# Optimization experiments

Hardware: AMD Instinct MI355X
Metric: run time of the kernel (lower is better)

The kernel has to match this reference:

```python
import jax, jax.numpy as jnp
import numpy as np

LN_EPS = 1e-5

def _ln(x, g, b):
    m = x.mean(-1, keepdims=True)
    v = ((x - m) ** 2).mean(-1, keepdims=True)
    return (x - m) / jnp.sqrt(v + LN_EPS) * g + b

def _mlp(x, W1, b1, g, beta, W2, b2):
    # Linear -> LayerNorm -> ReLU -> Linear
    h = jax.nn.relu(_ln(x @ W1 + b1, g, beta))
    return h @ W2 + b2

def setup_inputs() -> dict:
    key = jax.random.key(0)
    N, E, C_in, C_out, H = 50000, 800000, 64, 64, 64
    ks = jax.random.split(key, 16)
    def rn(k, shape, fan_in):
        return jax.random.normal(k, shape, jnp.float32) * (fan_in ** -0.5)
    return dict(
        x=jax.random.normal(ks[0], (N, C_in), jnp.float32),
        pos=jax.random.normal(ks[1], (N, 3), jnp.float32),
        edge_index=jax.random.randint(ks[2], (2, E), 0, N, jnp.int32),
        W_in=rn(ks[3], (C_in, C_in), C_in), b_in=jnp.zeros((C_in,), jnp.float32),
        W_lin=rn(ks[4], (C_in, C_out), C_in),
        W_src=rn(ks[5], (C_in, C_out), C_in),
        W_dst=rn(ks[6], (C_in, C_out), C_in),
        pos_W1=rn(ks[7], (3, H), 3), pos_b1=jnp.zeros((H,), jnp.float32),
        pos_g=jnp.ones((H,), jnp.float32), pos_beta=jnp.zeros((H,), jnp.float32),
        pos_W2=rn(ks[8], (H, C_out), H), pos_b2=jnp.zeros((C_out,), jnp.float32),
        att_W1=rn(ks[9], (C_out, H), C_out), att_b1=jnp.zeros((H,), jnp.float32),
        att_g=jnp.ones((H,), jnp.float32), att_beta=jnp.zeros((H,), jnp.float32),
        att_W2=rn(ks[10], (H, C_out), H), att_b2=jnp.zeros((C_out,), jnp.float32),
        W_out=rn(ks[11], (C_out, C_out), C_out), b_out=jnp.zeros((C_out,), jnp.float32),
    )

def reference(x, pos, edge_index, W_in, b_in, W_lin, W_src, W_dst,
              pos_W1, pos_b1, pos_g, pos_beta, pos_W2, pos_b2,
              att_W1, att_b1, att_g, att_beta, att_W2, att_b2,
              W_out, b_out):
    N = x.shape[0]
    # lin_in + relu
    x = jax.nn.relu(x @ W_in + b_in)
    # PointTransformerConv with add_self_loops=True (PyG default)
    loops = jnp.arange(N, dtype=edge_index.dtype)
    src = jnp.concatenate([edge_index[0], loops])  # j (neighbors)
    dst = jnp.concatenate([edge_index[1], loops])  # i (centers)
    a_src = x @ W_src           # [N, C_out]
    a_dst = x @ W_dst           # [N, C_out]
    v = x @ W_lin               # [N, C_out]
    # per-edge positional encoding delta = pos_nn(pos_i - pos_j)
    delta = _mlp(pos[dst] - pos[src], pos_W1, pos_b1, pos_g, pos_beta, pos_W2, pos_b2)  # [E, C_out]
    alpha = _mlp(a_dst[dst] - a_src[src] + delta, att_W1, att_b1, att_g, att_beta, att_W2, att_b2)
    # per-destination, per-channel softmax over variable-size neighborhoods
    amax = jax.ops.segment_max(alpha, dst, num_segments=N)
    e = jnp.exp(alpha - amax[dst])
    denom = jax.ops.segment_sum(e, dst, num_segments=N)
    w = e / jnp.clip(denom[dst], 1e-16)
    # weighted scatter-sum of (value_j + delta)
    out = jax.ops.segment_sum(w * (v[src] + delta), dst, num_segments=N)  # [N, C_out]
    # lin_out + relu
    return jax.nn.relu(out @ W_out + b_out)
```

## Files before the change

### kernel.cpp

```cpp
#include <hip/hip_runtime.h>
#include <hip/hip_bf16.h>


typedef __bf16 bf16x8 __attribute__((ext_vector_type(8)));
typedef short  s16x8  __attribute__((ext_vector_type(8)));
typedef float  f32x4  __attribute__((ext_vector_type(4)));

#define SWZ(b) ((b) ^ ((((b) >> 7) & 7) << 4))

__device__ __forceinline__ unsigned short f2b(float f) {
  union { __hip_bfloat16 h; unsigned short u; } c;
  c.h = __float2bfloat16(f);
  return c.u;
}
__device__ __forceinline__ unsigned int pack2(float a, float b) {
  return (unsigned int)f2b(a) | ((unsigned int)f2b(b) << 16);
}
__device__ __forceinline__ void lds_fence() {
  asm volatile("s_waitcnt lgkmcnt(0)" ::: "memory");
  __builtin_amdgcn_sched_barrier(0);
}

__device__ __forceinline__ void stage_wt(const float* __restrict__ W, char* dst, int tid) {
  for (int idx = tid; idx < 2048; idx += 256) {
    int c  = idx >> 5;
    int k2 = (idx & 31) << 1;
    float v0 = W[k2 * 64 + c];
    float v1 = W[(k2 + 1) * 64 + c];
    int byte = c * 128 + k2 * 2;
    *(unsigned int*)(dst + SWZ(byte)) = pack2(v0, v1);
  }
}

__device__ __forceinline__ void gemm16(const char* actb, const char* wb,
                                       int g, int m, f32x4 acc[4]) {
  #pragma unroll
  for (int kk = 0; kk < 2; kk++) {
    s16x8 af = *(const s16x8*)(actb + SWZ(m * 128 + g * 16 + kk * 64));
    #pragma unroll
    for (int t = 0; t < 4; t++) {
      s16x8 bf = *(const s16x8*)(wb + SWZ((t * 16 + m) * 128 + g * 16 + kk * 64));
      acc[t] = __builtin_amdgcn_mfma_f32_16x16x32_bf16(
          __builtin_bit_cast(bf16x8, af), __builtin_bit_cast(bf16x8, bf), acc[t], 0, 0, 0);
    }
  }
}

__global__ __launch_bounds__(256, 3) void node_mfma_kernel(
    const float* __restrict__ x,
    const float* __restrict__ W_in, const float* __restrict__ b_in,
    const float* __restrict__ W_lin, const float* __restrict__ W_src, const float* __restrict__ W_dst,
    float* __restrict__ a_src, float* __restrict__ a_dst, float* __restrict__ vv,
    int N)
{
  __shared__ __align__(16) char sWinT[8192], sWsT[8192], sWdT[8192], sWlT[8192], sX[8192];
  __shared__ float sB[64];
  int tid = threadIdx.x;
  stage_wt(W_in,  sWinT, tid);
  stage_wt(W_src, sWsT,  tid);
  stage_wt(W_dst, sWdT,  tid);
  stage_wt(W_lin, sWlT,  tid);
  if (tid < 64) sB[tid] = b_in[tid];

  const int lane = tid & 63, wv = tid >> 6;
  const int g = lane >> 4, m = lane & 15;
  const int ew = wv << 4;
  const int srow = tid >> 2, sc0 = (tid & 3) << 4;
  const int ntile = (N + 63) >> 6;

  for (int tile = blockIdx.x; tile < ntile; tile += gridDim.x) {
    const int rbase = tile << 6;
    __syncthreads();
    {
      int gr = rbase + srow; if (gr >= N) gr = N - 1;
      const float4* src = (const float4*)&x[(size_t)gr * 64 + sc0];
      #pragma unroll
      for (int q = 0; q < 4; q++) {
        float4 f = src[q];
        int byte = srow * 128 + sc0 * 2 + q * 8;
        *(unsigned int*)(sX + SWZ(byte))     = pack2(f.x, f.y);
        *(unsigned int*)(sX + SWZ(byte + 4)) = pack2(f.z, f.w);
      }
    }
    __syncthreads();

    f32x4 a0[4] = {};
    gemm16(sX + ew * 128, sWinT, g, m, a0);
    float x1[4][4];
    #pragma unroll
    for (int t = 0; t < 4; t++)
      #pragma unroll
      for (int r = 0; r < 4; r++) x1[t][r] = fmaxf(a0[t][r] + sB[t * 16 + m], 0.f);
    __syncthreads();
    #pragma unroll
    for (int t = 0; t < 4; t++)
      #pragma unroll
      for (int r = 0; r < 4; r++)
        *(unsigned short*)(sX + SWZ((ew + 4 * g + r) * 128 + (t * 16 + m) * 2)) = f2b(x1[t][r]);
    __syncthreads();

    f32x4 as[4] = {}, ad[4] = {}, al[4] = {};
    gemm16(sX + ew * 128, sWsT, g, m, as);
    gemm16(sX + ew * 128, sWdT, g, m, ad);
    gemm16(sX + ew * 128, sWlT, g, m, al);
    #pragma unroll
    for (int t = 0; t < 4; t++)
      #pragma unroll
      for (int r = 0; r < 4; r++) {
        int gr = rbase + ew + 4 * g + r;
        if (gr < N) {
          size_t o = (size_t)gr * 64 + t * 16 + m;
          a_src[o] = as[t][r]; a_dst[o] = ad[t][r]; vv[o] = al[t][r];
        }
      }
  }
}

__global__ void hist_kernel(const int* __restrict__ ei, int* __restrict__ deg, int E, int Etot) {
  int stride = gridDim.x * blockDim.x;
  for (int e = blockIdx.x * blockDim.x + threadIdx.x; e < Etot; e += stride) {
    int d = (e < E) ? ei[E + e] : (e - E);
    atomicAdd(&deg[d], 1);
  }
}

__global__ __launch_bounds__(256) void scanA_kernel(const int* __restrict__ deg, int* __restrict__ chunkSum, int N) {
  __shared__ int s[256];
  int i = blockIdx.x * 256 + threadIdx.x;
  s[threadIdx.x] = (i < N) ? deg[i] : 0;
  __syncthreads();
  for (int off = 128; off > 0; off >>= 1) {
    if (threadIdx.x < off) s[threadIdx.x] += s[threadIdx.x + off];
    __syncthreads();
  }
  if (threadIdx.x == 0) chunkSum[blockIdx.x] = s[0];
}

__global__ __launch_bounds__(256) void scanB_kernel(const int* __restrict__ chunkSum, int* __restrict__ chunkPre, int nchunk) {
  __shared__ int s[256];
  int t = threadIdx.x;
  int v = (t < nchunk) ? chunkSum[t] : 0;
  s[t] = v; __syncthreads();
  for (int off = 1; off < 256; off <<= 1) {
    int x = (t >= off) ? s[t - off] : 0;
    __syncthreads();
    s[t] += x;
    __syncthreads();
  }
  if (t < nchunk) chunkPre[t] = s[t] - v;
}

__global__ __launch_bounds__(256) void scanC_kernel(const int* __restrict__ deg, const int* __restrict__ chunkPre,
                                                    int* __restrict__ cursor, int N) {
  __shared__ int s[256];
  int t = threadIdx.x;
  int i = blockIdx.x * 256 + t;
  int v = (i < N) ? deg[i] : 0;
  s[t] = v; __syncthreads();
  for (int off = 1; off < 256; off <<= 1) {
    int x = (t >= off) ? s[t - off] : 0;
    __syncthreads();
    s[t] += x;
    __syncthreads();
  }
  if (i < N) cursor[i] = chunkPre[blockIdx.x] + s[t] - v;
}

__global__ void scatter_kernel(const int* __restrict__ ei, int* __restrict__ cursor,
                               const float* __restrict__ pos,
                               int* __restrict__ srcS, int* __restrict__ dstS,
                               float4* __restrict__ pd4,
                               int E, int Etot) {
  int stride = gridDim.x * blockDim.x;
  for (int e = blockIdx.x * blockDim.x + threadIdx.x; e < Etot; e += stride) {
    int s, d;
    if (e < E) { s = ei[e]; d = ei[E + e]; }
    else       { s = e - E; d = s; }
    int p = atomicAdd(&cursor[d], 1);
    srcS[p] = s; dstS[p] = d;
    float4 q;
    q.x = pos[d * 3 + 0] - pos[s * 3 + 0];
    q.y = pos[d * 3 + 1] - pos[s * 3 + 1];
    q.z = pos[d * 3 + 2] - pos[s * 3 + 2];
    q.w = 0.f;
    pd4[p] = q;
  }
}

__global__ __launch_bounds__(256, 3) void edge_kernel(
    const int* __restrict__ srcS, const int* __restrict__ dstS, const float4* __restrict__ pd4,
    const float* __restrict__ a_src_g, const float* __restrict__ a_dst_g, const float* __restrict__ v_g,
    const float* __restrict__ pos_W1, const float* __restrict__ pos_b1,
    const float* __restrict__ pos_gg, const float* __restrict__ pos_beta,
    const float* __restrict__ pos_W2, const float* __restrict__ pos_b2,
    const float* __restrict__ att_W1, const float* __restrict__ att_b1,
    const float* __restrict__ att_gg, const float* __restrict__ att_beta,
    const float* __restrict__ att_W2, const float* __restrict__ att_b2,
    float* __restrict__ numer, float* __restrict__ denom,
    int G, int gpw)
{
  __shared__ __align__(16) char sW2t[8192], sA1t[8192], sA2t[8192];
  __shared__ __align__(16) char sAct[4][2048];
  __shared__ float sAcc[4][4][128];
  __shared__ float sPW1[192];
  __shared__ float sPB1[64], sPG[64], sPBeta[64], sPB2[64];
  __shared__ float sAB1[64], sAG[64], sABeta[64], sAB2[64];

  int tid = threadIdx.x;
  stage_wt(pos_W2, sW2t, tid);
  stage_wt(att_W1, sA1t, tid);
  stage_wt(att_W2, sA2t, tid);
  for (int i = tid; i < 192; i += 256) sPW1[i] = pos_W1[i];
  if (tid < 64) {
    sPB1[tid] = pos_b1[tid]; sPG[tid] = pos_gg[tid]; sPBeta[tid] = pos_beta[tid]; sPB2[tid] = pos_b2[tid];
    sAB1[tid] = att_b1[tid]; sAG[tid] = att_gg[tid]; sABeta[tid] = att_beta[tid]; sAB2[tid] = att_b2[tid];
  }
  for (int i = tid; i < 4 * 4 * 128; i += 256) ((float*)sAcc)[i] = 0.f;
  __syncthreads();

  const int lane = tid & 63, wv = tid >> 6;
  const int g = lane >> 4, m = lane & 15;
  char* myAct = sAct[wv];
  float (*myAcc)[128] = sAcc[wv];

  const int w  = blockIdx.x * 4 + wv;
  const int g0 = w * gpw;
  int g1 = g0 + gpw; if (g1 > G) g1 = G;

  for (int grp = g0; grp < g1; ++grp) {
    const int ebase = grp << 4;

    float4 pdr[4];
    #pragma unroll
    for (int r = 0; r < 4; r++) pdr[r] = pd4[ebase + 4 * g + r];
    int dall[16];
    #pragma unroll
    for (int i = 0; i < 16; i++) dall[i] = dstS[ebase + i];
    int mys[4];
    #pragma unroll
    for (int r = 0; r < 4; r++) mys[r] = srcS[ebase + 4 * g + r];

    int myd[4] = {-1, -1, -1, -1};
    int sid_my[4] = {0, 0, 0, 0};
    int fd0 = dall[0], fd1 = -1, fd2 = -1, fd3 = -1;
    int cur = 0;
    #pragma unroll
    for (int i = 0; i < 16; i++) {
      if (i > 0) {
        bool b = (dall[i] != dall[i - 1]);
        cur += b ? 1 : 0;
        fd1 = (b && cur == 1) ? dall[i] : fd1;
        fd2 = (b && cur == 2) ? dall[i] : fd2;
        fd3 = (b && cur == 3) ? dall[i] : fd3;
      }
      bool mine = ((i >> 2) == g);
      const int rr = i & 3;
      if (rr == 0) { myd[0] = mine ? dall[i] : myd[0]; sid_my[0] = mine ? cur : sid_my[0]; }
      if (rr == 1) { myd[1] = mine ? dall[i] : myd[1]; sid_my[1] = mine ? cur : sid_my[1]; }
      if (rr == 2) { myd[2] = mine ? dall[i] : myd[2]; sid_my[2] = mine ? cur : sid_my[2]; }
      if (rr == 3) { myd[3] = mine ? dall[i] : myd[3]; sid_my[3] = mine ? cur : sid_my[3]; }
    }
    const int ns = cur + 1;

    float adst[16], asrc[16];
    #pragma unroll
    for (int r = 0; r < 4; r++) {
      int dm = myd[r] < 0 ? 0 : myd[r];
      int sm = mys[r];
      #pragma unroll
      for (int t = 0; t < 4; t++) {
        adst[r * 4 + t] = a_dst_g[(size_t)dm * 64 + t * 16 + m];
        asrc[r * 4 + t] = a_src_g[(size_t)sm * 64 + t * 16 + m];
      }
    }

    {
      float h[4][4];
      #pragma unroll
      for (int r = 0; r < 4; r++) {
        float p0 = pdr[r].x, p1 = pdr[r].y, p2 = pdr[r].z;
        #pragma unroll
        for (int t = 0; t < 4; t++) {
          int c = t * 16 + m;
          h[t][r] = fmaf(p0, sPW1[c], fmaf(p1, sPW1[64 + c], fmaf(p2, sPW1[128 + c], sPB1[c])));
        }
      }
      #pragma unroll
      for (int r = 0; r < 4; r++) {
        float s = h[0][r] + h[1][r] + h[2][r] + h[3][r];
        s += __shfl_xor(s, 1); s += __shfl_xor(s, 2); s += __shfl_xor(s, 4); s += __shfl_xor(s, 8);
        float mean = s * (1.f / 64.f);
        float q = 0.f;
        #pragma unroll
        for (int t = 0; t < 4; t++) { float dd = h[t][r] - mean; q = fmaf(dd, dd, q); }
        q += __shfl_xor(q, 1); q += __shfl_xor(q, 2); q += __shfl_xor(q, 4); q += __shfl_xor(q, 8);
        float rs = rsqrtf(q * (1.f / 64.f) + 1e-5f);
        #pragma unroll
        for (int t = 0; t < 4; t++) {
          int c = t * 16 + m;
          float val = fmaxf(fmaf((h[t][r] - mean) * rs, sPG[c], sPBeta[c]), 0.f);
          *(unsigned short*)(myAct + SWZ((4 * g + r) * 128 + c * 2)) = f2b(val);
        }
      }
    }
    lds_fence();

    f32x4 dacc[4] = {};
    gemm16(myAct, sW2t, g, m, dacc);
    float del[4][4];
    #pragma unroll
    for (int t = 0; t < 4; t++)
      #pragma unroll
      for (int r = 0; r < 4; r++) del[t][r] = dacc[t][r] + sPB2[t * 16 + m];
    lds_fence();

    float vv[16];
    #pragma unroll
    for (int r = 0; r < 4; r++)
      #pragma unroll
      for (int t = 0; t < 4; t++)
        vv[r * 4 + t] = v_g[(size_t)mys[r] * 64 + t * 16 + m];

    #pragma unroll
    for (int r = 0; r < 4; r++)
      #pragma unroll
      for (int t = 0; t < 4; t++) {
        float a = adst[r * 4 + t] - asrc[r * 4 + t] + del[t][r];
        *(unsigned short*)(myAct + SWZ((4 * g + r) * 128 + (t * 16 + m) * 2)) = f2b(a);
      }
    lds_fence();

    f32x4 acc2[4] = {};
    gemm16(myAct, sA1t, g, m, acc2);
    float h2[4][4];
    #pragma unroll
    for (int t = 0; t < 4; t++)
      #pragma unroll
      for (int r = 0; r < 4; r++) h2[t][r] = acc2[t][r] + sAB1[t * 16 + m];
    #pragma unroll
    for (int r = 0; r < 4; r++) {
      float s = h2[0][r] + h2[1][r] + h2[2][r] + h2[3][r];
      s += __shfl_xor(s, 1); s += __shfl_xor(s, 2); s += __shfl_xor(s, 4); s += __shfl_xor(s, 8);
      float mean = s * (1.f / 64.f);
      float q = 0.f;
      #pragma unroll
      for (int t = 0; t < 4; t++) { float dd = h2[t][r] - mean; q = fmaf(dd, dd, q); }
      q += __shfl_xor(q, 1); q += __shfl_xor(q, 2); q += __shfl_xor(q, 4); q += __shfl_xor(q, 8);
      float rs = rsqrtf(q * (1.f / 64.f) + 1e-5f);
      #pragma unroll
      for (int t = 0; t < 4; t++) {
        int c = t * 16 + m;
        h2[t][r] = fmaxf(fmaf((h2[t][r] - mean) * rs, sAG[c], sABeta[c]), 0.f);
      }
    }
    lds_fence();
    #pragma unroll
    for (int t = 0; t < 4; t++)
      #pragma unroll
      for (int r = 0; r < 4; r++)
        *(unsigned short*)(myAct + SWZ((4 * g + r) * 128 + (t * 16 + m) * 2)) = f2b(h2[t][r]);
    lds_fence();

    f32x4 acc3[4] = {};
    gemm16(myAct, sA2t, g, m, acc3);

    {
      float aN[4] = {0.f, 0.f, 0.f, 0.f}, aD[4] = {0.f, 0.f, 0.f, 0.f};
      int curS = -1, curD = 0;
      #pragma unroll
      for (int r = 0; r < 4; r++) {
        int d = myd[r];
        if (d < 0) continue;
        int sgid = sid_my[r];
        if (sgid != curS) {
          if (curS >= 0) {
            if (curS < 4) {
              #pragma unroll
              for (int t = 0; t < 4; t++) {
                atomicAdd(&myAcc[curS][t * 16 + m], aN[t]);
                atomicAdd(&myAcc[curS][64 + t * 16 + m], aD[t]);
              }
            } else {
              #pragma unroll
              for (int t = 0; t < 4; t++) {
                atomicAdd(&numer[(size_t)curD * 64 + t * 16 + m], aN[t]);
                atomicAdd(&denom[(size_t)curD * 64 + t * 16 + m], aD[t]);
              }
            }
          }
          curS = sgid; curD = d;
          #pragma unroll
          for (int t = 0; t < 4; t++) { aN[t] = 0.f; aD[t] = 0.f; }
        }
        #pragma unroll
        for (int t = 0; t < 4; t++) {
          float ee = __expf(acc3[t][r] + sAB2[t * 16 + m]);
          aN[t] = fmaf(ee, vv[r * 4 + t] + del[t][r], aN[t]);
          aD[t] += ee;
        }
      }
      if (curS >= 0) {
        if (curS < 4) {
          #pragma unroll
          for (int t = 0; t < 4; t++) {
            atomicAdd(&myAcc[curS][t * 16 + m], aN[t]);
            atomicAdd(&myAcc[curS][64 + t * 16 + m], aD[t]);
          }
        } else {
          #pragma unroll
          for (int t = 0; t < 4; t++) {
            atomicAdd(&numer[(size_t)curD * 64 + t * 16 + m], aN[t]);
            atomicAdd(&denom[(size_t)curD * 64 + t * 16 + m], aD[t]);
          }
        }
      }
    }
    lds_fence();

    {
      const int nsc = ns < 4 ? ns : 4;
      const int fdk[1] = {0}; (void)fdk;
      #pragma unroll
      for (int k = 0; k < 4; k++) {
        int dd = (k == 0) ? fd0 : (k == 1) ? fd1 : (k == 2) ? fd2 : fd3;
        if (k < nsc && dd >= 0) {
          float nv = myAcc[k][lane];
          float dv = myAcc[k][64 + lane];
          atomicAdd(&numer[(size_t)dd * 64 + lane], nv);
          atomicAdd(&denom[(size_t)dd * 64 + lane], dv);
          myAcc[k][lane] = 0.f;
          myAcc[k][64 + lane] = 0.f;
        }
      }
    }
    lds_fence();
  }
}

__global__ __launch_bounds__(256) void out_mfma_kernel(
    const float* __restrict__ numer, const float* __restrict__ denom,
    const float* __restrict__ W_out, const float* __restrict__ b_out,
    float* __restrict__ out, int N)
{
  __shared__ __align__(16) char sWoT[8192], sX[8192];
  __shared__ float sB[64];
  int tid = threadIdx.x;
  stage_wt(W_out, sWoT, tid);
  if (tid < 64) sB[tid] = b_out[tid];

  const int lane = tid & 63, wv = tid >> 6;
  const int g = lane >> 4, m = lane & 15;
  const int ew = wv << 4;
  const int srow = tid >> 2, sc0 = (tid & 3) << 4;
  const int ntile = (N + 63) >> 6;

  for (int tile = blockIdx.x; tile < ntile; tile += gridDim.x) {
    const int rbase = tile << 6;
    __syncthreads();
    {
      int gr = rbase + srow; if (gr >= N) gr = N - 1;
      const float4* nsrc = (const float4*)&numer[(size_t)gr * 64 + sc0];
      const float4* dsrc = (const float4*)&denom[(size_t)gr * 64 + sc0];
      #pragma unroll
      for (int q = 0; q < 4; q++) {
        float4 fn = nsrc[q], fd = dsrc[q];
        float m0 = fn.x / fmaxf(fd.x, 1e-16f);
        float m1 = fn.y / fmaxf(fd.y, 1e-16f);
        float m2 = fn.z / fmaxf(fd.z, 1e-16f);
        float m3 = fn.w / fmaxf(fd.w, 1e-16f);
        int byte = srow * 128 + sc0 * 2 + q * 8;
        *(unsigned int*)(sX + SWZ(byte))     = pack2(m0, m1);
        *(unsigned int*)(sX + SWZ(byte + 4)) = pack2(m2, m3);
      }
    }
    __syncthreads();
    f32x4 acc[4] = {};
    gemm16(sX + ew * 128, sWoT, g, m, acc);
    #pragma unroll
    for (int t = 0; t < 4; t++)
      #pragma unroll
      for (int r = 0; r < 4; r++) {
        int gr = rbase + ew + 4 * g + r;
        if (gr < N) out[(size_t)gr * 64 + t * 16 + m] = fmaxf(acc[t][r] + sB[t * 16 + m], 0.f);
      }
  }
}

extern "C" void kernel_launch(void* const* d_in, const int* in_sizes, int n_in,
                              void* d_out, int out_size, void* d_ws, size_t ws_size,
                              hipStream_t stream) {
  (void)n_in; (void)out_size; (void)ws_size;
  const float* x        = (const float*)d_in[0];
  const float* pos      = (const float*)d_in[1];
  const int*   ei       = (const int*)  d_in[2];
  const float* W_in     = (const float*)d_in[3];
  const float* b_in     = (const float*)d_in[4];
  const float* W_lin    = (const float*)d_in[5];
  const float* W_src    = (const float*)d_in[6];
  const float* W_dst    = (const float*)d_in[7];
  const float* pos_W1   = (const float*)d_in[8];
  const float* pos_b1   = (const float*)d_in[9];
  const float* pos_g    = (const float*)d_in[10];
  const float* pos_beta = (const float*)d_in[11];
  const float* pos_W2   = (const float*)d_in[12];
  const float* pos_b2   = (const float*)d_in[13];
  const float* att_W1   = (const float*)d_in[14];
  const float* att_b1   = (const float*)d_in[15];
  const float* att_g    = (const float*)d_in[16];
  const float* att_beta = (const float*)d_in[17];
  const float* att_W2   = (const float*)d_in[18];
  const float* att_b2   = (const float*)d_in[19];
  const float* W_out    = (const float*)d_in[20];
  const float* b_out    = (const float*)d_in[21];

  const int N    = in_sizes[0] / 64;
  const int E    = in_sizes[2] / 2;
  const int Etot = E + N;
  const int Epad = (Etot + 15) & ~15;
  const size_t N64 = (size_t)N * 64;

  float* a_src = (float*)d_ws;
  float* a_dst = a_src + N64;
  float* v     = a_dst + N64;
  float* numer = v + N64;
  float* denom = numer + N64;
  int* deg      = (int*)(denom + N64);
  int* cursor   = deg + N;
  int* chunkSum = cursor + N;
  int* chunkPre = chunkSum + 256;
  int* srcS     = chunkPre + 256;
  int* dstS     = srcS + Epad;
  float4* pd4   = (float4*)(dstS + Epad);

  const int nchunk = (N + 255) / 256;

  hipMemsetAsync(deg, 0, (size_t)N * sizeof(int), stream);
  hipMemsetAsync(numer, 0, 2 * N64 * sizeof(float), stream);
  if (Epad > Etot) {
    hipMemsetAsync(dstS + Etot, 0xFF, (size_t)(Epad - Etot) * sizeof(int), stream);
    hipMemsetAsync(srcS + Etot, 0, (size_t)(Epad - Etot) * sizeof(int), stream);
    hipMemsetAsync(pd4 + Etot, 0, (size_t)(Epad - Etot) * sizeof(float4), stream);
  }

  hist_kernel<<<1024, 256, 0, stream>>>(ei, deg, E, Etot);
  scanA_kernel<<<nchunk, 256, 0, stream>>>(deg, chunkSum, N);
  scanB_kernel<<<1, 256, 0, stream>>>(chunkSum, chunkPre, nchunk);
  scanC_kernel<<<nchunk, 256, 0, stream>>>(deg, chunkPre, cursor, N);
  scatter_kernel<<<1024, 256, 0, stream>>>(ei, cursor, pos, srcS, dstS, pd4, E, Etot);

  const int ntileN = (N + 63) / 64;
  const int nblkN  = ntileN < 768 ? ntileN : 768;
  node_mfma_kernel<<<nblkN, 256, 0, stream>>>(x, W_in, b_in, W_lin, W_src, W_dst,
                                              a_src, a_dst, v, N);

  const int G   = Epad / 16;
  const int NB  = 768;
  const int gpw = (G + NB * 4 - 1) / (NB * 4);
  edge_kernel<<<NB, 256, 0, stream>>>(srcS, dstS, pd4, a_src, a_dst, v,
      pos_W1, pos_b1, pos_g, pos_beta, pos_W2, pos_b2,
      att_W1, att_b1, att_g, att_beta, att_W2, att_b2,
      numer, denom, G, gpw);

  out_mfma_kernel<<<nblkN, 256, 0, stream>>>(numer, denom, W_out, b_out, (float*)d_out, N);
}
```

Before: 482.2 us.

## Store node features in bf16 and run edge MLPs in registers via transposed MFMA

Node projections a_src, a_dst and v are now written as bf16, which halves the bytes gathered per edge. The edge kernel swaps the MFMA operands so each lane owns one edge. That lets the activations stay in registers between the three GEMMs, using permuted weight staging, and removes the per-wave LDS activation buffers and fences. Segment reduction now uses a DPP segmented scan within 16-lane rows, with atomics issued only from segment tails, replacing the LDS accumulator scheme. The costs are reduced precision on the gathered features and more global atomics per edge group.

```diff
diff --git a/kernel.cpp b/kernel.cpp
--- a/kernel.cpp
+++ b/kernel.cpp
@@ -5,6 +5,8 @@
 typedef __bf16 bf16x8 __attribute__((ext_vector_type(8)));
 typedef short  s16x8  __attribute__((ext_vector_type(8)));
 typedef float  f32x4  __attribute__((ext_vector_type(4)));
+
+union B8 { s16x8 v; unsigned int u[4]; };
 
 #define SWZ(b) ((b) ^ ((((b) >> 7) & 7) << 4))
 
@@ -16,19 +18,40 @@
 __device__ __forceinline__ unsigned int pack2(float a, float b) {
   return (unsigned int)f2b(a) | ((unsigned int)f2b(b) << 16);
 }
-__device__ __forceinline__ void lds_fence() {
-  asm volatile("s_waitcnt lgkmcnt(0)" ::: "memory");
-  __builtin_amdgcn_sched_barrier(0);
+__device__ __forceinline__ void unpack2(unsigned int u, float& a, float& b) {
+  union { unsigned int x; float f; } t0, t1;
+  t0.x = u << 16; t1.x = u & 0xffff0000u;
+  a = t0.f; b = t1.f;
+}
+
+template <int CTRL>
+__device__ __forceinline__ float dppf(float x) {
+  return __builtin_bit_cast(float,
+      __builtin_amdgcn_update_dpp(0, __builtin_bit_cast(int, x), CTRL, 0xF, 0xF, false));
+}
+template <int CTRL>
+__device__ __forceinline__ int dppi(int x, int old) {
+  return __builtin_amdgcn_update_dpp(old, x, CTRL, 0xF, 0xF, false);
+}
+
+__device__ __forceinline__ int lmap(int q) {
+  int kk = q >> 5, gg = (q >> 3) & 3, j = q & 7;
+  return 32 * kk + 16 * (j >> 2) + 4 * gg + (j & 3);
 }
 
 __device__ __forceinline__ void stage_wt(const float* __restrict__ W, char* dst, int tid) {
   for (int idx = tid; idx < 2048; idx += 256) {
     int c  = idx >> 5;
     int k2 = (idx & 31) << 1;
-    float v0 = W[k2 * 64 + c];
-    float v1 = W[(k2 + 1) * 64 + c];
-    int byte = c * 128 + k2 * 2;
-    *(unsigned int*)(dst + SWZ(byte)) = pack2(v0, v1);
+    *(unsigned int*)(dst + SWZ(c * 128 + k2 * 2)) = pack2(W[k2 * 64 + c], W[(k2 + 1) * 64 + c]);
+  }
+}
+__device__ __forceinline__ void stage_wt_perm(const float* __restrict__ W, char* dst, int tid) {
+  for (int idx = tid; idx < 2048; idx += 256) {
+    int c  = idx >> 5;
+    int k2 = (idx & 31) << 1;
+    *(unsigned int*)(dst + SWZ(c * 128 + k2 * 2)) =
+        pack2(W[lmap(k2) * 64 + c], W[lmap(k2 + 1) * 64 + c]);
   }
 }
 
@@ -50,8 +73,8 @@
     const float* __restrict__ x,
     const float* __restrict__ W_in, const float* __restrict__ b_in,
     const float* __restrict__ W_lin, const float* __restrict__ W_src, const float* __restrict__ W_dst,
-    float* __restrict__ a_src, float* __restrict__ a_dst, float* __restrict__ vv,
-    int N)
+    unsigned short* __restrict__ a_srcB, unsigned short* __restrict__ a_dstB,
+    unsigned short* __restrict__ vB, int N)
 {
   __shared__ __align__(16) char sWinT[8192], sWsT[8192], sWdT[8192], sWlT[8192], sX[8192];
   __shared__ float sB[64];
@@ -110,7 +133,7 @@
         int gr = rbase + ew + 4 * g + r;
         if (gr < N) {
           size_t o = (size_t)gr * 64 + t * 16 + m;
-          a_src[o] = as[t][r]; a_dst[o] = ad[t][r]; vv[o] = al[t][r];
+          a_srcB[o] = f2b(as[t][r]); a_dstB[o] = f2b(ad[t][r]); vB[o] = f2b(al[t][r]);
         }
       }
   }
@@ -189,7 +212,8 @@
 
 __global__ __launch_bounds__(256, 3) void edge_kernel(
     const int* __restrict__ srcS, const int* __restrict__ dstS, const float4* __restrict__ pd4,
-    const float* __restrict__ a_src_g, const float* __restrict__ a_dst_g, const float* __restrict__ v_g,
+    const unsigned short* __restrict__ a_srcB, const unsigned short* __restrict__ a_dstB,
+    const unsigned short* __restrict__ vBg,
     const float* __restrict__ pos_W1, const float* __restrict__ pos_b1,
     const float* __restrict__ pos_gg, const float* __restrict__ pos_beta,
     const float* __restrict__ pos_W2, const float* __restrict__ pos_b2,
@@ -200,240 +224,241 @@
     int G, int gpw)
 {
   __shared__ __align__(16) char sW2t[8192], sA1t[8192], sA2t[8192];
-  __shared__ __align__(16) char sAct[4][2048];
-  __shared__ float sAcc[4][4][128];
   __shared__ float sPW1[192];
   __shared__ float sPB1[64], sPG[64], sPBeta[64], sPB2[64];
   __shared__ float sAB1[64], sAG[64], sABeta[64], sAB2[64];
 
   int tid = threadIdx.x;
   stage_wt(pos_W2, sW2t, tid);
-  stage_wt(att_W1, sA1t, tid);
-  stage_wt(att_W2, sA2t, tid);
+  stage_wt_perm(att_W1, sA1t, tid);
+  stage_wt_perm(att_W2, sA2t, tid);
   for (int i = tid; i < 192; i += 256) sPW1[i] = pos_W1[i];
   if (tid < 64) {
     sPB1[tid] = pos_b1[tid]; sPG[tid] = pos_gg[tid]; sPBeta[tid] = pos_beta[tid]; sPB2[tid] = pos_b2[tid];
     sAB1[tid] = att_b1[tid]; sAG[tid] = att_gg[tid]; sABeta[tid] = att_beta[tid]; sAB2[tid] = att_b2[tid];
   }
-  for (int i = tid; i < 4 * 4 * 128; i += 256) ((float*)sAcc)[i] = 0.f;
   __syncthreads();
 
-  const int lane = tid & 63, wv = tid >> 6;
+  const int lane = tid & 63;
   const int g = lane >> 4, m = lane & 15;
-  char* myAct = sAct[wv];
-  float (*myAcc)[128] = sAcc[wv];
-
-  const int w  = blockIdx.x * 4 + wv;
+
+  const int w  = blockIdx.x * 4 + (tid >> 6);
   const int g0 = w * gpw;
   int g1 = g0 + gpw; if (g1 > G) g1 = G;
 
   for (int grp = g0; grp < g1; ++grp) {
     const int ebase = grp << 4;
 
-    float4 pdr[4];
-    #pragma unroll
-    for (int r = 0; r < 4; r++) pdr[r] = pd4[ebase + 4 * g + r];
-    int dall[16];
-    #pragma unroll
-    for (int i = 0; i < 16; i++) dall[i] = dstS[ebase + i];
-    int mys[4];
-    #pragma unroll
-    for (int r = 0; r < 4; r++) mys[r] = srcS[ebase + 4 * g + r];
-
-    int myd[4] = {-1, -1, -1, -1};
-    int sid_my[4] = {0, 0, 0, 0};
-    int fd0 = dall[0], fd1 = -1, fd2 = -1, fd3 = -1;
-    int cur = 0;
-    #pragma unroll
-    for (int i = 0; i < 16; i++) {
-      if (i > 0) {
-        bool b = (dall[i] != dall[i - 1]);
-        cur += b ? 1 : 0;
-        fd1 = (b && cur == 1) ? dall[i] : fd1;
-        fd2 = (b && cur == 2) ? dall[i] : fd2;
-        fd3 = (b && cur == 3) ? dall[i] : fd3;
-      }
-      bool mine = ((i >> 2) == g);
-      const int rr = i & 3;
-      if (rr == 0) { myd[0] = mine ? dall[i] : myd[0]; sid_my[0] = mine ? cur : sid_my[0]; }
-      if (rr == 1) { myd[1] = mine ? dall[i] : myd[1]; sid_my[1] = mine ? cur : sid_my[1]; }
-      if (rr == 2) { myd[2] = mine ? dall[i] : myd[2]; sid_my[2] = mine ? cur : sid_my[2]; }
-      if (rr == 3) { myd[3] = mine ? dall[i] : myd[3]; sid_my[3] = mine ? cur : sid_my[3]; }
-    }
-    const int ns = cur + 1;
-
-    float adst[16], asrc[16];
-    #pragma unroll
-    for (int r = 0; r < 4; r++) {
-      int dm = myd[r] < 0 ? 0 : myd[r];
-      int sm = mys[r];
+    int d = dstS[ebase + m];
+    int sN = srcS[ebase + m];
+    f32x4 pd = *(const f32x4*)&pd4[ebase + m];
+    const bool valid = d >= 0;
+    const int dm = valid ? d : 0;
+
+    int dprev = dppi<0x111>(d, -1);
+    int dnext = dppi<0x101>(d, -1);
+    bool head = (d != dprev);
+    bool tl   = (d != dnext);
+    unsigned long long hb = __ballot(head);
+    unsigned mask16 = (unsigned)(hb >> (g * 16)) & 0xFFFFu;
+    unsigned maskLE = mask16 & ((1u << (m + 1)) - 1u);
+    int hd = m - (31 - __builtin_clz(maskLE | 1u));
+
+    uint2 AD[2][2], AS[2][2], VV[4];
+    #pragma unroll
+    for (int kk = 0; kk < 2; kk++)
+      #pragma unroll
+      for (int h = 0; h < 2; h++) {
+        int c0 = 32 * kk + 16 * h + 4 * g;
+        AD[kk][h] = *(const uint2*)&a_dstB[(size_t)dm * 64 + c0];
+        AS[kk][h] = *(const uint2*)&a_srcB[(size_t)sN * 64 + c0];
+      }
+    #pragma unroll
+    for (int t = 0; t < 4; t++)
+      VV[t] = *(const uint2*)&vBg[(size_t)sN * 64 + 16 * t + 4 * g];
+
+    float u[2][8];
+    #pragma unroll
+    for (int kk = 0; kk < 2; kk++)
+      #pragma unroll
+      for (int h = 0; h < 2; h++) {
+        int q = 8 * g + 32 * kk + 4 * h;
+        f32x4 w0 = *(const f32x4*)&sPW1[q];
+        f32x4 w1 = *(const f32x4*)&sPW1[64 + q];
+        f32x4 w2 = *(const f32x4*)&sPW1[128 + q];
+        f32x4 bb = *(const f32x4*)&sPB1[q];
+        #pragma unroll
+        for (int r = 0; r < 4; r++)
+          u[kk][4 * h + r] = fmaf(pd[0], w0[r], fmaf(pd[1], w1[r], fmaf(pd[2], w2[r], bb[r])));
+      }
+    {
+      float s1 = 0.f;
+      #pragma unroll
+      for (int kk = 0; kk < 2; kk++)
+        #pragma unroll
+        for (int j = 0; j < 8; j++) s1 += u[kk][j];
+      s1 += __shfl_xor(s1, 16); s1 += __shfl_xor(s1, 32);
+      float mean = s1 * (1.f / 64.f);
+      float qv = 0.f;
+      #pragma unroll
+      for (int kk = 0; kk < 2; kk++)
+        #pragma unroll
+        for (int j = 0; j < 8; j++) { float dd = u[kk][j] - mean; qv = fmaf(dd, dd, qv); }
+      qv += __shfl_xor(qv, 16); qv += __shfl_xor(qv, 32);
+      float rs = rsqrtf(qv * (1.f / 64.f) + 1e-5f);
+      #pragma unroll
+      for (int kk = 0; kk < 2; kk++)
+        #pragma unroll
+        for (int h = 0; h < 2; h++) {
+          int q = 8 * g + 32 * kk + 4 * h;
+          f32x4 gg4 = *(const f32x4*)&sPG[q];
+          f32x4 bt4 = *(const f32x4*)&sPBeta[q];
+          #pragma unroll
+          for (int r = 0; r < 4; r++)
+            u[kk][4 * h + r] = fmaxf(fmaf((u[kk][4 * h + r] - mean) * rs, gg4[r], bt4[r]), 0.f);
+        }
+    }
+    B8 bA[2];
+    #pragma unroll
+    for (int kk = 0; kk < 2; kk++)
+      #pragma unroll
+      for (int p = 0; p < 4; p++)
+        bA[kk].u[p] = pack2(u[kk][2 * p], u[kk][2 * p + 1]);
+
+    f32x4 del[4] = {};
+    #pragma unroll
+    for (int kk = 0; kk < 2; kk++)
       #pragma unroll
       for (int t = 0; t < 4; t++) {
-        adst[r * 4 + t] = a_dst_g[(size_t)dm * 64 + t * 16 + m];
-        asrc[r * 4 + t] = a_src_g[(size_t)sm * 64 + t * 16 + m];
-      }
-    }
-
+        s16x8 wf = *(const s16x8*)(sW2t + SWZ((t * 16 + m) * 128 + g * 16 + kk * 64));
+        del[t] = __builtin_amdgcn_mfma_f32_16x16x32_bf16(
+            __builtin_bit_cast(bf16x8, wf), __builtin_bit_cast(bf16x8, bA[kk].v), del[t], 0, 0, 0);
+      }
+    #pragma unroll
+    for (int t = 0; t < 4; t++) {
+      f32x4 b2 = *(const f32x4*)&sPB2[16 * t + 4 * g];
+      #pragma unroll
+      for (int r = 0; r < 4; r++) del[t][r] += b2[r];
+    }
+
+    B8 bT[2];
+    #pragma unroll
+    for (int kk = 0; kk < 2; kk++)
+      #pragma unroll
+      for (int h = 0; h < 2; h++) {
+        float a0, a1, a2, a3, b0, b1, b2v, b3;
+        unpack2(AD[kk][h].x, a0, a1); unpack2(AD[kk][h].y, a2, a3);
+        unpack2(AS[kk][h].x, b0, b1); unpack2(AS[kk][h].y, b2v, b3);
+        int t = 2 * kk + h;
+        float e0 = a0 - b0 + del[t][0];
+        float e1 = a1 - b1 + del[t][1];
+        float e2 = a2 - b2v + del[t][2];
+        float e3 = a3 - b3 + del[t][3];
+        bT[kk].u[2 * h]     = pack2(e0, e1);
+        bT[kk].u[2 * h + 1] = pack2(e2, e3);
+      }
+
+    f32x4 acc2[4] = {};
+    #pragma unroll
+    for (int kk = 0; kk < 2; kk++)
+      #pragma unroll
+      for (int t = 0; t < 4; t++) {
+        s16x8 wf = *(const s16x8*)(sA1t + SWZ((t * 16 + m) * 128 + g * 16 + kk * 64));
+        acc2[t] = __builtin_amdgcn_mfma_f32_16x16x32_bf16(
+            __builtin_bit_cast(bf16x8, wf), __builtin_bit_cast(bf16x8, bT[kk].v), acc2[t], 0, 0, 0);
+      }
+    float h2[4][4];
+    #pragma unroll
+    for (int t = 0; t < 4; t++) {
+      f32x4 ab1 = *(const f32x4*)&sAB1[16 * t + 4 * g];
+      #pragma unroll
+      for (int r = 0; r < 4; r++) h2[t][r] = acc2[t][r] + ab1[r];
+    }
     {
-      float h[4][4];
+      float s1 = 0.f;
+      #pragma unroll
+      for (int t = 0; t < 4; t++)
+        #pragma unroll
+        for (int r = 0; r < 4; r++) s1 += h2[t][r];
+      s1 += __shfl_xor(s1, 16); s1 += __shfl_xor(s1, 32);
+      float mean = s1 * (1.f / 64.f);
+      float qv = 0.f;
+      #pragma unroll
+      for (int t = 0; t < 4; t++)
+        #pragma unroll
+        for (int r = 0; r < 4; r++) { float dd = h2[t][r] - mean; qv = fmaf(dd, dd, qv); }
+      qv += __shfl_xor(qv, 16); qv += __shfl_xor(qv, 32);
+      float rs = rsqrtf(qv * (1.f / 64.f) + 1e-5f);
+      #pragma unroll
+      for (int t = 0; t < 4; t++) {
+        f32x4 gg4 = *(const f32x4*)&sAG[16 * t + 4 * g];
+        f32x4 bt4 = *(const f32x4*)&sABeta[16 * t + 4 * g];
+        #pragma unroll
+        for (int r = 0; r < 4; r++)
+          h2[t][r] = fmaxf(fmaf((h2[t][r] - mean) * rs, gg4[r], bt4[r]), 0.f);
+      }
+    }
+    B8 bH[2];
+    #pragma unroll
+    for (int kk = 0; kk < 2; kk++) {
+      bH[kk].u[0] = pack2(h2[2 * kk][0], h2[2 * kk][1]);
+      bH[kk].u[1] = pack2(h2[2 * kk][2], h2[2 * kk][3]);
+      bH[kk].u[2] = pack2(h2[2 * kk + 1][0], h2[2 * kk + 1][1]);
+      bH[kk].u[3] = pack2(h2[2 * kk + 1][2], h2[2 * kk + 1][3]);
+    }
+
+    f32x4 acc3[4] = {};
+    #pragma unroll
+    for (int kk = 0; kk < 2; kk++)
+      #pragma unroll
+      for (int t = 0; t < 4; t++) {
+        s16x8 wf = *(const s16x8*)(sA2t + SWZ((t * 16 + m) * 128 + g * 16 + kk * 64));
+        acc3[t] = __builtin_amdgcn_mfma_f32_16x16x32_bf16(
+            __builtin_bit_cast(bf16x8, wf), __builtin_bit_cast(bf16x8, bH[kk].v), acc3[t], 0, 0, 0);
+      }
+
+    f32x4 aN[4], aD[4];
+    #pragma unroll
+    for (int t = 0; t < 4; t++) {
+      f32x4 ab2 = *(const f32x4*)&sAB2[16 * t + 4 * g];
+      float v0, v1, v2, v3;
+      unpack2(VV[t].x, v0, v1); unpack2(VV[t].y, v2, v3);
+      float vr[4] = {v0, v1, v2, v3};
       #pragma unroll
       for (int r = 0; r < 4; r++) {
-        float p0 = pdr[r].x, p1 = pdr[r].y, p2 = pdr[r].z;
-        #pragma unroll
-        for (int t = 0; t < 4; t++) {
-          int c = t * 16 + m;
-          h[t][r] = fmaf(p0, sPW1[c], fmaf(p1, sPW1[64 + c], fmaf(p2, sPW1[128 + c], sPB1[c])));
+        float e = __expf(acc3[t][r] + ab2[r]);
+        e = valid ? e : 0.f;
+        aN[t][r] = e * (vr[r] + del[t][r]);
+        aD[t][r] = e;
+      }
+    }
+    #define SCAN_ROUND(OFF, CTRL)                                        \
+      { bool p = hd >= OFF;                                              \
+        _Pragma("unroll")                                                \
+        for (int t = 0; t < 4; t++) {                                    \
+          _Pragma("unroll")                                              \
+          for (int r = 0; r < 4; r++) {                                  \
+            float shN = dppf<CTRL>(aN[t][r]);                            \
+            float shD = dppf<CTRL>(aD[t][r]);                            \
+            aN[t][r] += p ? shN : 0.f;                                   \
+            aD[t][r] += p ? shD : 0.f;                                   \
+          }                                                              \
+        } }
+    SCAN_ROUND(1, 0x111)
+    SCAN_ROUND(2, 0x112)
+    SCAN_ROUND(4, 0x114)
+    SCAN_ROUND(8, 0x118)
+    #undef SCAN_ROUND
+
+    if (valid && tl) {
+      #pragma unroll
+      for (int t = 0; t < 4; t++)
+        #pragma unroll
+        for (int r = 0; r < 4; r++) {
+          atomicAdd(&numer[(size_t)d * 64 + 16 * t + 4 * g + r], aN[t][r]);
+          atomicAdd(&denom[(size_t)d * 64 + 16 * t + 4 * g + r], aD[t][r]);
         }
-      }
-      #pragma unroll
-      for (int r = 0; r < 4; r++) {
-        float s = h[0][r] + h[1][r] + h[2][r] + h[3][r];
-        s += __shfl_xor(s, 1); s += __shfl_xor(s, 2); s += __shfl_xor(s, 4); s += __shfl_xor(s, 8);
-        float mean = s * (1.f / 64.f);
-        float q = 0.f;
-        #pragma unroll
-        for (int t = 0; t < 4; t++) { float dd = h[t][r] - mean; q = fmaf(dd, dd, q); }
-        q += __shfl_xor(q, 1); q += __shfl_xor(q, 2); q += __shfl_xor(q, 4); q += __shfl_xor(q, 8);
-        float rs = rsqrtf(q * (1.f / 64.f) + 1e-5f);
-        #pragma unroll
-        for (int t = 0; t < 4; t++) {
-          int c = t * 16 + m;
-          float val = fmaxf(fmaf((h[t][r] - mean) * rs, sPG[c], sPBeta[c]), 0.f);
-          *(unsigned short*)(myAct + SWZ((4 * g + r) * 128 + c * 2)) = f2b(val);
-        }
-      }
-    }
-    lds_fence();
-
-    f32x4 dacc[4] = {};
-    gemm16(myAct, sW2t, g, m, dacc);
-    float del[4][4];
-    #pragma unroll
-    for (int t = 0; t < 4; t++)
-      #pragma unroll
-      for (int r = 0; r < 4; r++) del[t][r] = dacc[t][r] + sPB2[t * 16 + m];
-    lds_fence();
-
-    float vv[16];
-    #pragma unroll
-    for (int r = 0; r < 4; r++)
-      #pragma unroll
-      for (int t = 0; t < 4; t++)
-        vv[r * 4 + t] = v_g[(size_t)mys[r] * 64 + t * 16 + m];
-
-    #pragma unroll
-    for (int r = 0; r < 4; r++)
-      #pragma unroll
-      for (int t = 0; t < 4; t++) {
-        float a = adst[r * 4 + t] - asrc[r * 4 + t] + del[t][r];
-        *(unsigned short*)(myAct + SWZ((4 * g + r) * 128 + (t * 16 + m) * 2)) = f2b(a);
-      }
-    lds_fence();
-
-    f32x4 acc2[4] = {};
-    gemm16(myAct, sA1t, g, m, acc2);
-    float h2[4][4];
-    #pragma unroll
-    for (int t = 0; t < 4; t++)
-      #pragma unroll
-      for (int r = 0; r < 4; r++) h2[t][r] = acc2[t][r] + sAB1[t * 16 + m];
-    #pragma unroll
-    for (int r = 0; r < 4; r++) {
-      float s = h2[0][r] + h2[1][r] + h2[2][r] + h2[3][r];
-      s += __shfl_xor(s, 1); s += __shfl_xor(s, 2); s += __shfl_xor(s, 4); s += __shfl_xor(s, 8);
-      float mean = s * (1.f / 64.f);
-      float q = 0.f;
-      #pragma unroll
-      for (int t = 0; t < 4; t++) { float dd = h2[t][r] - mean; q = fmaf(dd, dd, q); }
-      q += __shfl_xor(q, 1); q += __shfl_xor(q, 2); q += __shfl_xor(q, 4); q += __shfl_xor(q, 8);
-      float rs = rsqrtf(q * (1.f / 64.f) + 1e-5f);
-      #pragma unroll
-      for (int t = 0; t < 4; t++) {
-        int c = t * 16 + m;
-        h2[t][r] = fmaxf(fmaf((h2[t][r] - mean) * rs, sAG[c], sABeta[c]), 0.f);
-      }
-    }
-    lds_fence();
-    #pragma unroll
-    for (int t = 0; t < 4; t++)
-      #pragma unroll
-      for (int r = 0; r < 4; r++)
-        *(unsigned short*)(myAct + SWZ((4 * g + r) * 128 + (t * 16 + m) * 2)) = f2b(h2[t][r]);
-    lds_fence();
-
-    f32x4 acc3[4] = {};
-    gemm16(myAct, sA2t, g, m, acc3);
-
-    {
-      float aN[4] = {0.f, 0.f, 0.f, 0.f}, aD[4] = {0.f, 0.f, 0.f, 0.f};
-      int curS = -1, curD = 0;
-      #pragma unroll
-      for (int r = 0; r < 4; r++) {
-        int d = myd[r];
-        if (d < 0) continue;
-        int sgid = sid_my[r];
-        if (sgid != curS) {
-          if (curS >= 0) {
-            if (curS < 4) {
-              #pragma unroll
-              for (int t = 0; t < 4; t++) {
-                atomicAdd(&myAcc[curS][t * 16 + m], aN[t]);
-                atomicAdd(&myAcc[curS][64 + t * 16 + m], aD[t]);
-              }
-            } else {
-              #pragma unroll
-              for (int t = 0; t < 4; t++) {
-                atomicAdd(&numer[(size_t)curD * 64 + t * 16 + m], aN[t]);
-                atomicAdd(&denom[(size_t)curD * 64 + t * 16 + m], aD[t]);
-              }
-            }
-          }
-          curS = sgid; curD = d;
-          #pragma unroll
-          for (int t = 0; t < 4; t++) { aN[t] = 0.f; aD[t] = 0.f; }
-        }
-        #pragma unroll
-        for (int t = 0; t < 4; t++) {
-          float ee = __expf(acc3[t][r] + sAB2[t * 16 + m]);
-          aN[t] = fmaf(ee, vv[r * 4 + t] + del[t][r], aN[t]);
-          aD[t] += ee;
-        }
-      }
-      if (curS >= 0) {
-        if (curS < 4) {
-          #pragma unroll
-          for (int t = 0; t < 4; t++) {
-            atomicAdd(&myAcc[curS][t * 16 + m], aN[t]);
-            atomicAdd(&myAcc[curS][64 + t * 16 + m], aD[t]);
-          }
-        } else {
-          #pragma unroll
-          for (int t = 0; t < 4; t++) {
-            atomicAdd(&numer[(size_t)curD * 64 + t * 16 + m], aN[t]);
-            atomicAdd(&denom[(size_t)curD * 64 + t * 16 + m], aD[t]);
-          }
-        }
-      }
-    }
-    lds_fence();
-
-    {
-      const int nsc = ns < 4 ? ns : 4;
-      const int fdk[1] = {0}; (void)fdk;
-      #pragma unroll
-      for (int k = 0; k < 4; k++) {
-        int dd = (k == 0) ? fd0 : (k == 1) ? fd1 : (k == 2) ? fd2 : fd3;
-        if (k < nsc && dd >= 0) {
-          float nv = myAcc[k][lane];
-          float dv = myAcc[k][64 + lane];
-          atomicAdd(&numer[(size_t)dd * 64 + lane], nv);
-          atomicAdd(&denom[(size_t)dd * 64 + lane], dv);
-          myAcc[k][lane] = 0.f;
-          myAcc[k][64 + lane] = 0.f;
-        }
-      }
-    }
-    lds_fence();
+    }
   }
 }
 
@@ -519,18 +544,18 @@
   const int Epad = (Etot + 15) & ~15;
   const size_t N64 = (size_t)N * 64;
 
-  float* a_src = (float*)d_ws;
-  float* a_dst = a_src + N64;
-  float* v     = a_dst + N64;
-  float* numer = v + N64;
+  float* numer = (float*)d_ws;
   float* denom = numer + N64;
-  int* deg      = (int*)(denom + N64);
+  unsigned short* aSb = (unsigned short*)(denom + N64);
+  unsigned short* aDb = aSb + N64;
+  unsigned short* vBb = aDb + N64;
+  float4* pd4 = (float4*)(vBb + N64);
+  int* srcS     = (int*)(pd4 + Epad);
+  int* dstS     = srcS + Epad;
+  int* deg      = dstS + Epad;
   int* cursor   = deg + N;
   int* chunkSum = cursor + N;
   int* chunkPre = chunkSum + 256;
-  int* srcS     = chunkPre + 256;
-  int* dstS     = srcS + Epad;
-  float4* pd4   = (float4*)(dstS + Epad);
 
   const int nchunk = (N + 255) / 256;
 
@@ -551,12 +576,12 @@
   const int ntileN = (N + 63) / 64;
   const int nblkN  = ntileN < 768 ? ntileN : 768;
   node_mfma_kernel<<<nblkN, 256, 0, stream>>>(x, W_in, b_in, W_lin, W_src, W_dst,
-                                              a_src, a_dst, v, N);
+                                              aSb, aDb, vBb, N);
 
   const int G   = Epad / 16;
   const int NB  = 768;
   const int gpw = (G + NB * 4 - 1) / (NB * 4);
-  edge_kernel<<<NB, 256, 0, stream>>>(srcS, dstS, pd4, a_src, a_dst, v,
+  edge_kernel<<<NB, 256, 0, stream>>>(srcS, dstS, pd4, aSb, aDb, vBb,
       pos_W1, pos_b1, pos_g, pos_beta, pos_W2, pos_b2,
       att_W1, att_b1, att_g, att_beta, att_W2, att_b2,
       numer, denom, G, gpw);
```

Result: slower. 640.1 us (+32.7%).
